# Performance work log

Measured on AMD Instinct MI355X. Metric: run time of the kernel, lower is better.

## Reference

```python
import jax, jax.numpy as jnp
import numpy as np

SIGMA = 1.0
RADIUS = 4        # int(truncate * sigma + 0.5), skimage default truncate=4.0
NBINS = 256       # skimage threshold_otsu default
MEAN, STD = 0.5, 0.5


def _gauss_kernel():
    xs = np.arange(-RADIUS, RADIUS + 1, dtype=np.float32)
    k = np.exp(-0.5 * (xs / SIGMA) ** 2)
    return jnp.asarray(k / k.sum())


def _blur(img):
    # img: [B, H, W]; skimage gaussian(sigma=1) == separable conv, 'nearest' (edge) padding
    k = _gauss_kernel()
    p = jnp.pad(img, ((0, 0), (RADIUS, RADIUS), (RADIUS, RADIUS)), mode='edge')
    x = p[:, None]  # [B,1,H+2R,W+2R]
    x = jax.lax.conv_general_dilated(x, k.reshape(1, 1, -1, 1), (1, 1), 'VALID')
    x = jax.lax.conv_general_dilated(x, k.reshape(1, 1, 1, -1), (1, 1), 'VALID')
    return x[:, 0]


def _otsu(img):
    # Otsu threshold over a 256-bin histogram spanning [min, max] (skimage semantics)
    mn, mx = img.min(), img.max()
    rng = jnp.maximum(mx - mn, 1e-12)
    idx = jnp.clip(jnp.floor((img - mn) / rng * NBINS).astype(jnp.int32), 0, NBINS - 1)
    hist = jnp.zeros(NBINS, jnp.float32).at[idx.ravel()].add(1.0)
    centers = mn + (jnp.arange(NBINS, dtype=jnp.float32) + 0.5) * (rng / NBINS)
    w1 = jnp.cumsum(hist)
    w2 = jnp.cumsum(hist[::-1])[::-1]
    m1 = jnp.cumsum(hist * centers) / jnp.maximum(w1, 1e-12)
    m2 = jnp.cumsum((hist * centers)[::-1])[::-1] / jnp.maximum(w2, 1e-12)
    var12 = w1[:-1] * w2[1:] * (m1[:-1] - m2[1:]) ** 2
    return centers[jnp.argmax(var12)]


def setup_inputs() -> dict:
    key = jax.random.key(0)
    x = jax.random.normal(key, (32, 4, 512, 512), dtype=jnp.float32)
    return {"x": x}


def reference(x):
    # thershold_mask on thermal channel: denormalize (mul std, add mean), clamp, blur, Otsu
    thermal = jnp.clip(x[:, 0] * STD + MEAN, 0.0, 1.0)          # [B,H,W]
    blurred = _blur(thermal)                                     # [B,H,W]
    t = jax.vmap(_otsu)(blurred)                                 # [B]
    mask = jnp.where(blurred > t[:, None, None], 1.0, blurred)   # soft mask
    # rgba2rgb with white background: out = alpha*rgb + (1-alpha)*1, clipped to [0,1]
    rgb = x[:, -3:]                                              # [B,3,H,W]
    alpha = mask[:, None]                                        # [B,1,H,W]
    out_rgb = jnp.clip(alpha * rgb + (1.0 - alpha), 0.0, 1.0)
    # use_thermal=True: replace last 3 channels, keep thermal channel
    return x.at[:, 1:4].set(out_rgb)
```

## Files before the change

kernel.cpp:

```cpp
#include <hip/hip_runtime.h>
#include <math.h>

#define NIMG 32
#define HWDIM 512
#define NPIX (HWDIM * HWDIM)
#define NB 256
#define RAD 4
#define TW 64
#define TH 64

struct W9 { float w[9]; };

__device__ __forceinline__ float clip01(float v) { return fminf(fmaxf(v, 0.0f), 1.0f); }

static float np_expf(float x) {
  const float LOG2E = 1.442695040f;
  const float CW_HI = -6.93145752e-1f;
  const float CW_LO = -1.42860677e-6f;
  const float P0 = 9.999999999980870924916e-01f;
  const float P1 = 7.257664613233124478488e-01f;
  const float P2 = 2.473615434895520810817e-01f;
  const float P3 = 5.114512081637298353406e-02f;
  const float P4 = 6.757896990527504603057e-03f;
  const float P5 = 5.082762527590693718096e-04f;
  const float Q0 = 1.000000000000000000000e+00f;
  const float Q1 = -2.742335390411667452936e-01f;
  const float Q2 = 2.159509375685829852307e-02f;
  float m = rintf(x * LOG2E);
  float y = fmaf(m, CW_HI, x);
  y = fmaf(m, CW_LO, y);
  float num = fmaf(fmaf(fmaf(fmaf(fmaf(P5, y, P4), y, P3), y, P2), y, P1), y, P0);
  float den = fmaf(fmaf(Q2, y, Q1), y, Q0);
  float r = num / den;
  return ldexpf(r, (int)m);
}

__global__ __launch_bounds__(256) void init_kernel(int* __restrict__ minI, int* __restrict__ maxI,
                                                   int* __restrict__ hist) {
  int tid = blockIdx.x * blockDim.x + threadIdx.x;
  if (tid < NIMG) { minI[tid] = 0x7F800000; maxI[tid] = 0; }
  int stride = gridDim.x * blockDim.x;
  for (int i = tid; i < NIMG * NB; i += stride) hist[i] = 0;
}

__global__ __launch_bounds__(256) void blur_kernel(const float* __restrict__ x, float* __restrict__ out,
                                                   int* __restrict__ minI, int* __restrict__ maxI, W9 wp) {
  __shared__ float raw[TH + 8][TW + 8];
  __shared__ float vb[TH][TW + 8];
  const int img = blockIdx.z;
  const int tx0 = blockIdx.x * TW;
  const int ty0 = blockIdx.y * TH;
  const float* src = x + (size_t)img * 4 * NPIX;
  float* out0 = out + (size_t)img * 4 * NPIX;
  float* bl = out0 + NPIX;
  const int tid = threadIdx.x;

  for (int i = tid; i < (TH + 8) * (TW + 8); i += 256) {
    int lr = i / (TW + 8), lc = i % (TW + 8);
    int gr = ty0 - RAD + lr; gr = gr < 0 ? 0 : (gr > HWDIM - 1 ? HWDIM - 1 : gr);
    int gc = tx0 - RAD + lc; gc = gc < 0 ? 0 : (gc > HWDIM - 1 ? HWDIM - 1 : gc);
    float v = src[gr * HWDIM + gc];
    if (lr >= RAD && lr < RAD + TH && lc >= RAD && lc < RAD + TW)
      out0[gr * HWDIM + gc] = v;
    raw[lr][lc] = clip01(__fadd_rn(__fmul_rn(v, 0.5f), 0.5f));
  }
  __syncthreads();

  for (int i = tid; i < TH * (TW + 8); i += 256) {
    int r = i / (TW + 8), c = i % (TW + 8);
    double acc = 0.0;
#pragma unroll
    for (int k = 0; k < 9; ++k) acc += (double)wp.w[k] * (double)raw[r + k][c];
    vb[r][c] = (float)acc;
  }
  __syncthreads();

  float lmn = __int_as_float(0x7F800000);
  float lmx = 0.0f;
  for (int i = tid; i < TH * TW; i += 256) {
    int r = i >> 6, c = i & 63;
    double acc = 0.0;
#pragma unroll
    for (int k = 0; k < 9; ++k) acc += (double)wp.w[k] * (double)vb[r][c + k];
    float a = (float)acc;
    bl[(ty0 + r) * HWDIM + (tx0 + c)] = a;
    lmn = fminf(lmn, a);
    lmx = fmaxf(lmx, a);
  }
  for (int off = 32; off > 0; off >>= 1) {
    lmn = fminf(lmn, __shfl_down(lmn, off, 64));
    lmx = fmaxf(lmx, __shfl_down(lmx, off, 64));
  }
  __shared__ float smn[4], smx[4];
  if ((tid & 63) == 0) { smn[tid >> 6] = lmn; smx[tid >> 6] = lmx; }
  __syncthreads();
  if (tid == 0) {
    float mnb = fminf(fminf(smn[0], smn[1]), fminf(smn[2], smn[3]));
    float mxb = fmaxf(fmaxf(smx[0], smx[1]), fmaxf(smx[2], smx[3]));
    atomicMin(&minI[img], __float_as_int(mnb));
    atomicMax(&maxI[img], __float_as_int(mxb));
  }
}

__global__ __launch_bounds__(256) void hist_kernel(const float* __restrict__ out, const int* __restrict__ minI,
                                                   const int* __restrict__ maxI, int* __restrict__ hist) {
  __shared__ int lh[4 * 260];
  const int img = blockIdx.y;
  const int tid = threadIdx.x;
  for (int i = tid; i < 4 * 260; i += 256) lh[i] = 0;
  __syncthreads();
  const float mn = __int_as_float(minI[img]);
  const float mx = __int_as_float(maxI[img]);
  const float rng = fmaxf(mx - mn, 1e-12f);
  const float4* src = (const float4*)(out + (size_t)img * 4 * NPIX + NPIX);
  int* my = lh + (tid & 3) * 260;
#pragma unroll
  for (int j = 0; j < 4; ++j) {
    float4 v = src[blockIdx.x * 1024 + j * 256 + tid];
    float q; int b;
    q = __fmul_rn(__fdiv_rn(__fsub_rn(v.x, mn), rng), 256.0f); b = (int)floorf(q); b = b < 0 ? 0 : (b > 255 ? 255 : b); atomicAdd(&my[b], 1);
    q = __fmul_rn(__fdiv_rn(__fsub_rn(v.y, mn), rng), 256.0f); b = (int)floorf(q); b = b < 0 ? 0 : (b > 255 ? 255 : b); atomicAdd(&my[b], 1);
    q = __fmul_rn(__fdiv_rn(__fsub_rn(v.z, mn), rng), 256.0f); b = (int)floorf(q); b = b < 0 ? 0 : (b > 255 ? 255 : b); atomicAdd(&my[b], 1);
    q = __fmul_rn(__fdiv_rn(__fsub_rn(v.w, mn), rng), 256.0f); b = (int)floorf(q); b = b < 0 ? 0 : (b > 255 ? 255 : b); atomicAdd(&my[b], 1);
  }
  __syncthreads();
  int c = lh[tid] + lh[260 + tid] + lh[2 * 260 + tid] + lh[3 * 260 + tid];
  if (c) atomicAdd(&hist[img * NB + tid], c);
}

__global__ __launch_bounds__(64) void otsu_kernel(const int* __restrict__ hist, const int* __restrict__ minI,
                                                  const int* __restrict__ maxI, float* __restrict__ t) {
  __shared__ float rs[NIMG][NB + 1];
  const int tid = threadIdx.x;
  if (tid >= NIMG) return;
  const int* h = hist + tid * NB;
  const float mn = __int_as_float(minI[tid]);
  const float mx = __int_as_float(maxI[tid]);
  const float rng = fmaxf(mx - mn, 1e-12f);
  const float scale = rng / 256.0f;

  float acc = 0.0f;
  rs[tid][NB] = 0.0f;
  for (int i = NB - 1; i >= 0; --i) {
    float c = __fadd_rn(mn, __fmul_rn((float)i + 0.5f, scale));
    float hc = __fmul_rn((float)h[i], c);
    acc = __fadd_rn(acc, hc);
    rs[tid][i] = acc;
  }

  float w1 = 0.0f, cs1 = 0.0f, best = -INFINITY;
  int arg = 0;
  for (int i = 0; i < NB - 1; ++i) {
    float hi = (float)h[i];
    float c = __fadd_rn(mn, __fmul_rn((float)i + 0.5f, scale));
    w1 = __fadd_rn(w1, hi);
    cs1 = __fadd_rn(cs1, __fmul_rn(hi, c));
    float w2n = (float)NPIX - w1;
    float m1 = __fdiv_rn(cs1, fmaxf(w1, 1e-12f));
    float m2n = __fdiv_rn(rs[tid][i + 1], fmaxf(w2n, 1e-12f));
    float d = __fsub_rn(m1, m2n);
    float v = __fmul_rn(__fmul_rn(w1, w2n), __fmul_rn(d, d));
    if (v > best) { best = v; arg = i; }
  }
  t[tid] = __fadd_rn(mn, __fmul_rn((float)arg + 0.5f, scale));
}

__global__ __launch_bounds__(256) void mask_kernel(const float* __restrict__ x, const float* __restrict__ tarr,
                                                   float* __restrict__ out) {
  const int gid = blockIdx.x * 256 + threadIdx.x;
  const int img = gid >> 16;
  const int rem = gid & 65535;
  const float4* xb = (const float4*)(x + (size_t)img * 4 * NPIX);
  float4* ob = (float4*)(out + (size_t)img * 4 * NPIX);
  const float tv = tarr[img];

  float4 bl = ob[65536 + rem];
  float4 x1 = xb[65536 + rem];
  float4 x2 = xb[2 * 65536 + rem];
  float4 x3 = xb[3 * 65536 + rem];

  float a0 = bl.x > tv ? 1.0f : bl.x;
  float a1 = bl.y > tv ? 1.0f : bl.y;
  float a2 = bl.z > tv ? 1.0f : bl.z;
  float a3 = bl.w > tv ? 1.0f : bl.w;

  float4 o1, o2, o3;
  o1.x = clip01(__fadd_rn(__fmul_rn(a0, x1.x), 1.0f - a0));
  o1.y = clip01(__fadd_rn(__fmul_rn(a1, x1.y), 1.0f - a1));
  o1.z = clip01(__fadd_rn(__fmul_rn(a2, x1.z), 1.0f - a2));
  o1.w = clip01(__fadd_rn(__fmul_rn(a3, x1.w), 1.0f - a3));
  o2.x = clip01(__fadd_rn(__fmul_rn(a0, x2.x), 1.0f - a0));
  o2.y = clip01(__fadd_rn(__fmul_rn(a1, x2.y), 1.0f - a1));
  o2.z = clip01(__fadd_rn(__fmul_rn(a2, x2.z), 1.0f - a2));
  o2.w = clip01(__fadd_rn(__fmul_rn(a3, x2.w), 1.0f - a3));
  o3.x = clip01(__fadd_rn(__fmul_rn(a0, x3.x), 1.0f - a0));
  o3.y = clip01(__fadd_rn(__fmul_rn(a1, x3.y), 1.0f - a1));
  o3.z = clip01(__fadd_rn(__fmul_rn(a2, x3.z), 1.0f - a2));
  o3.w = clip01(__fadd_rn(__fmul_rn(a3, x3.w), 1.0f - a3));

  ob[65536 + rem] = o1;
  ob[2 * 65536 + rem] = o2;
  ob[3 * 65536 + rem] = o3;
}

extern "C" void kernel_launch(void* const* d_in, const int* in_sizes, int n_in,
                              void* d_out, int out_size, void* d_ws, size_t ws_size,
                              hipStream_t stream) {
  const float* x = (const float*)d_in[0];
  float* out = (float*)d_out;
  char* ws = (char*)d_ws;
  int* minI = (int*)(ws + 0);
  int* maxI = (int*)(ws + 128);
  int* hist = (int*)(ws + 256);
  float* t = (float*)(ws + 256 + NIMG * NB * 4);

  W9 wp;
  {
    float k[9];
    for (int i = 0; i < 9; ++i) {
      float xs = (float)(i - 4);
      float argv = -0.5f * (xs * xs);
      k[i] = np_expf(argv);
    }
    float s = ((k[0] + k[1]) + (k[2] + k[3])) + ((k[4] + k[5]) + (k[6] + k[7]));
    s = s + k[8];
    for (int i = 0; i < 9; ++i) wp.w[i] = k[i] / s;
  }

  hipLaunchKernelGGL(init_kernel, dim3(33), dim3(256), 0, stream, minI, maxI, hist);
  hipLaunchKernelGGL(blur_kernel, dim3(HWDIM / TW, HWDIM / TH, NIMG), dim3(256), 0, stream,
                     x, out, minI, maxI, wp);
  hipLaunchKernelGGL(hist_kernel, dim3(NPIX / 16 / 256, NIMG), dim3(256), 0, stream,
                     out, minI, maxI, hist);
  hipLaunchKernelGGL(otsu_kernel, dim3(1), dim3(64), 0, stream, hist, minI, maxI, t);
  hipLaunchKernelGGL(mask_kernel, dim3(NIMG * NPIX / 4 / 256), dim3(256), 0, stream,
                     x, t, out);
}
```

Before: 137.6 us.

## Fuse Otsu threshold into histogram kernel via last-block completion counter

Removes the separate single-block Otsu launch. Each image's histogram blocks bump a per-image atomic counter, and the last block to finish reloads the global histogram and computes that image's threshold. This runs the 32 images' Otsu scans in parallel across blocks instead of in 32 lanes of one block. It also widens the privatized shared histograms from 4 to 16 copies to cut atomic contention, at the cost of more shared memory and a longer reduction.

Measured after the change: 224.4 us. +63.1%, slower.

```diff
diff --git a/kernel.cpp b/kernel.cpp
--- a/kernel.cpp
+++ b/kernel.cpp
@@ -36,9 +36,9 @@
 }
 
 __global__ __launch_bounds__(256) void init_kernel(int* __restrict__ minI, int* __restrict__ maxI,
-                                                   int* __restrict__ hist) {
+                                                   int* __restrict__ hist, int* __restrict__ cnt) {
   int tid = blockIdx.x * blockDim.x + threadIdx.x;
-  if (tid < NIMG) { minI[tid] = 0x7F800000; maxI[tid] = 0; }
+  if (tid < NIMG) { minI[tid] = 0x7F800000; maxI[tid] = 0; cnt[tid] = 0; }
   int stride = gridDim.x * blockDim.x;
   for (int i = tid; i < NIMG * NB; i += stride) hist[i] = 0;
 }
@@ -102,18 +102,20 @@
   }
 }
 
-__global__ __launch_bounds__(256) void hist_kernel(const float* __restrict__ out, const int* __restrict__ minI,
-                                                   const int* __restrict__ maxI, int* __restrict__ hist) {
-  __shared__ int lh[4 * 260];
+__global__ __launch_bounds__(256) void histotsu_kernel(const float* __restrict__ out, const int* __restrict__ minI,
+                                                       const int* __restrict__ maxI, int* __restrict__ hist,
+                                                       int* __restrict__ cnt, float* __restrict__ t) {
+  __shared__ int lh[16 * 257];
+  __shared__ int isLast;
   const int img = blockIdx.y;
   const int tid = threadIdx.x;
-  for (int i = tid; i < 4 * 260; i += 256) lh[i] = 0;
+  for (int i = tid; i < 16 * 257; i += 256) lh[i] = 0;
   __syncthreads();
   const float mn = __int_as_float(minI[img]);
   const float mx = __int_as_float(maxI[img]);
   const float rng = fmaxf(mx - mn, 1e-12f);
   const float4* src = (const float4*)(out + (size_t)img * 4 * NPIX + NPIX);
-  int* my = lh + (tid & 3) * 260;
+  int* my = lh + (tid & 15) * 257;
 #pragma unroll
   for (int j = 0; j < 4; ++j) {
     float4 v = src[blockIdx.x * 1024 + j * 256 + tid];
@@ -124,45 +126,48 @@
     q = __fmul_rn(__fdiv_rn(__fsub_rn(v.w, mn), rng), 256.0f); b = (int)floorf(q); b = b < 0 ? 0 : (b > 255 ? 255 : b); atomicAdd(&my[b], 1);
   }
   __syncthreads();
-  int c = lh[tid] + lh[260 + tid] + lh[2 * 260 + tid] + lh[3 * 260 + tid];
+  int c = 0;
+#pragma unroll
+  for (int s = 0; s < 16; ++s) c += lh[s * 257 + tid];
   if (c) atomicAdd(&hist[img * NB + tid], c);
-}
-
-__global__ __launch_bounds__(64) void otsu_kernel(const int* __restrict__ hist, const int* __restrict__ minI,
-                                                  const int* __restrict__ maxI, float* __restrict__ t) {
-  __shared__ float rs[NIMG][NB + 1];
-  const int tid = threadIdx.x;
-  if (tid >= NIMG) return;
-  const int* h = hist + tid * NB;
-  const float mn = __int_as_float(minI[tid]);
-  const float mx = __int_as_float(maxI[tid]);
-  const float rng = fmaxf(mx - mn, 1e-12f);
+
+  if (tid == 0) {
+    __threadfence();
+    int prev = atomicAdd(&cnt[img], 1);
+    isLast = (prev == gridDim.x - 1) ? 1 : 0;
+  }
+  __syncthreads();
+  if (!isLast) return;
+
+  lh[tid] = __hip_atomic_load(&hist[img * NB + tid], __ATOMIC_RELAXED, __HIP_MEMORY_SCOPE_AGENT);
+  __syncthreads();
+  if (tid != 0) return;
+
+  const int* h = lh;
+  float* rs = (float*)(lh + 320);
   const float scale = rng / 256.0f;
-
   float acc = 0.0f;
-  rs[tid][NB] = 0.0f;
+  rs[NB] = 0.0f;
   for (int i = NB - 1; i >= 0; --i) {
-    float c = __fadd_rn(mn, __fmul_rn((float)i + 0.5f, scale));
-    float hc = __fmul_rn((float)h[i], c);
-    acc = __fadd_rn(acc, hc);
-    rs[tid][i] = acc;
-  }
-
+    float cc = __fadd_rn(mn, __fmul_rn((float)i + 0.5f, scale));
+    acc = __fadd_rn(acc, __fmul_rn((float)h[i], cc));
+    rs[i] = acc;
+  }
   float w1 = 0.0f, cs1 = 0.0f, best = -INFINITY;
   int arg = 0;
   for (int i = 0; i < NB - 1; ++i) {
     float hi = (float)h[i];
-    float c = __fadd_rn(mn, __fmul_rn((float)i + 0.5f, scale));
+    float cc = __fadd_rn(mn, __fmul_rn((float)i + 0.5f, scale));
     w1 = __fadd_rn(w1, hi);
-    cs1 = __fadd_rn(cs1, __fmul_rn(hi, c));
+    cs1 = __fadd_rn(cs1, __fmul_rn(hi, cc));
     float w2n = (float)NPIX - w1;
     float m1 = __fdiv_rn(cs1, fmaxf(w1, 1e-12f));
-    float m2n = __fdiv_rn(rs[tid][i + 1], fmaxf(w2n, 1e-12f));
+    float m2n = __fdiv_rn(rs[i + 1], fmaxf(w2n, 1e-12f));
     float d = __fsub_rn(m1, m2n);
     float v = __fmul_rn(__fmul_rn(w1, w2n), __fmul_rn(d, d));
     if (v > best) { best = v; arg = i; }
   }
-  t[tid] = __fadd_rn(mn, __fmul_rn((float)arg + 0.5f, scale));
+  t[img] = __fadd_rn(mn, __fmul_rn((float)arg + 0.5f, scale));
 }
 
 __global__ __launch_bounds__(256) void mask_kernel(const float* __restrict__ x, const float* __restrict__ tarr,
@@ -213,6 +218,7 @@
   int* maxI = (int*)(ws + 128);
   int* hist = (int*)(ws + 256);
   float* t = (float*)(ws + 256 + NIMG * NB * 4);
+  int* cnt = (int*)(ws + 256 + NIMG * NB * 4 + NIMG * 4);
 
   W9 wp;
   {
@@ -227,12 +233,11 @@
     for (int i = 0; i < 9; ++i) wp.w[i] = k[i] / s;
   }
 
-  hipLaunchKernelGGL(init_kernel, dim3(33), dim3(256), 0, stream, minI, maxI, hist);
+  hipLaunchKernelGGL(init_kernel, dim3(33), dim3(256), 0, stream, minI, maxI, hist, cnt);
   hipLaunchKernelGGL(blur_kernel, dim3(HWDIM / TW, HWDIM / TH, NIMG), dim3(256), 0, stream,
                      x, out, minI, maxI, wp);
-  hipLaunchKernelGGL(hist_kernel, dim3(NPIX / 16 / 256, NIMG), dim3(256), 0, stream,
-                     out, minI, maxI, hist);
-  hipLaunchKernelGGL(otsu_kernel, dim3(1), dim3(64), 0, stream, hist, minI, maxI, t);
+  hipLaunchKernelGGL(histotsu_kernel, dim3(NPIX / 16 / 256, NIMG), dim3(256), 0, stream,
+                     out, minI, maxI, hist, cnt, t);
   hipLaunchKernelGGL(mask_kernel, dim3(NIMG * NPIX / 4 / 256), dim3(256), 0, stream,
                      x, t, out);
 }
```
